# Optimization experiments

Measured on AMD Instinct MI355X. Metric: run time of the kernel, lower is better.

The kernel has to match this reference:

```python
import jax, jax.numpy as jnp
import numpy as np

E = 1024
H = 16
D = E // H  # head_dim = 64
B = 2
S = 2048


def setup_inputs() -> dict:
    key = jax.random.key(0)
    ks = jax.random.split(key, 8)
    sc = 0.02
    return {
        "x": jax.random.normal(ks[0], (B, S, E), jnp.float32),
        "rotation_params": jax.random.normal(ks[1], (E, E), jnp.float32) * sc,
        "entangle_params": jax.random.normal(ks[2], (E, E), jnp.float32) * sc,
        "qkv_w": jax.random.normal(ks[3], (3 * E, E), jnp.float32) * sc,
        "qkv_b": jax.random.normal(ks[4], (3 * E,), jnp.float32) * sc,
        "out_w": jax.random.normal(ks[5], (E, E), jnp.float32) * sc,
        "out_b": jax.random.normal(ks[6], (E,), jnp.float32) * sc,
    }


def reference(x, rotation_params, entangle_params, qkv_w, qkv_b, out_w, out_b):
    b, s, _ = x.shape
    # qkv projection (torch Linear: x @ W.T + b)
    qkv = jnp.einsum('bse,fe->bsf', x, qkv_w) + qkv_b
    q, k, v = jnp.split(qkv, 3, axis=-1)
    # extra rotation / entangle matmuls on q and k
    q = jnp.matmul(q, rotation_params)
    k = jnp.matmul(k, entangle_params)
    # split heads: (b, h, s, d)
    q = q.reshape(b, s, H, D).transpose(0, 2, 1, 3)
    k = k.reshape(b, s, H, D).transpose(0, 2, 1, 3)
    v = v.reshape(b, s, H, D).transpose(0, 2, 1, 3)
    scores = jnp.einsum('bhqd,bhkd->bhqk', q, k) / np.sqrt(D).astype(np.float32)
    attn = jax.nn.softmax(scores, axis=-1)  # dropout p=0.0 -> identity
    out = jnp.einsum('bhqk,bhkd->bhqd', attn, v)
    out = out.transpose(0, 2, 1, 3).reshape(b, s, E)
    out = jnp.einsum('bse,fe->bsf', out, out_w) + out_b
    return out + x
```

## Files before the change

kernel.cpp:

```cpp
#include <hip/hip_runtime.h>

#define US unsigned short
#define UC unsigned char

typedef __bf16 bf16x8 __attribute__((ext_vector_type(8)));
typedef float f32x4 __attribute__((ext_vector_type(4)));
typedef unsigned int u32x4 __attribute__((ext_vector_type(4)));
typedef unsigned short u16x4 __attribute__((ext_vector_type(4)));
typedef unsigned int uint2v __attribute__((ext_vector_type(2)));

#define ALPHA_Q 0.180336880111f

#if __has_builtin(__builtin_amdgcn_exp2f)
#define EXP2F(x) __builtin_amdgcn_exp2f(x)
#else
#define EXP2F(x) __expf(0.69314718f * (x))
#endif

static __device__ __forceinline__ US f2bf(float f) {
    union { float f; unsigned u; } v; v.f = f;
    unsigned r = v.u + 0x7fffu + ((v.u >> 16) & 1u);
    return (US)(r >> 16);
}
static __device__ __forceinline__ float bf2f(US h) {
    union { unsigned u; float f; } v; v.u = ((unsigned)h) << 16;
    return v.f;
}
static __device__ __forceinline__ f32x4 mfma16(bf16x8 a, bf16x8 b, f32x4 c) {
    return __builtin_amdgcn_mfma_f32_16x16x32_bf16(a, b, c, 0, 0, 0);
}
static __device__ __forceinline__ f32x4 mfma_fp8(long long a, long long b, f32x4 c) {
    return __builtin_amdgcn_mfma_f32_16x16x32_fp8_fp8(a, b, c, 0, 0, 0);
}
static __device__ __forceinline__ void gload16(const US* g, US* l) {
    __builtin_amdgcn_global_load_lds(
        (const __attribute__((address_space(1))) void*)g,
        (__attribute__((address_space(3))) void*)l, 16, 0, 0);
}
static __device__ __forceinline__ void gload16b(const UC* g, UC* l) {
    __builtin_amdgcn_global_load_lds(
        (const __attribute__((address_space(1))) void*)g,
        (__attribute__((address_space(3))) void*)l, 16, 0, 0);
}
static __device__ __forceinline__ void stf(float* p, float v) { *p = v; }
static __device__ __forceinline__ void stf(US* p, float v) { *p = f2bf(v); }

__global__ __launch_bounds__(256) void prep(
    const float* __restrict__ x, US* __restrict__ xb,
    const float* __restrict__ qkvw, US* __restrict__ wv,
    const float* __restrict__ outw, US* __restrict__ wo,
    const float* __restrict__ Rm, US* __restrict__ rt,
    const float* __restrict__ Em, US* __restrict__ et,
    US* __restrict__ wqT, US* __restrict__ wkT,
    const float* __restrict__ qkvb, float* __restrict__ b3)
{
    __shared__ float t[64][65];
    const int bx = blockIdx.x;
    if (bx < 6144) {
        int i = bx * 256 + threadIdx.x;
        const float* s; US* d; int j;
        if (i < 1048576) { s = x; d = xb; j = i; }
        else if (i < 1310720) { s = qkvw + (size_t)2048 * 1024; d = wv; j = i - 1048576; }
        else { s = outw; d = wo; j = i - 1310720; }
        f32x4 v = ((const f32x4*)s)[j];
        u16x4 o;
        o.x = f2bf(v.x); o.y = f2bf(v.y); o.z = f2bf(v.z); o.w = f2bf(v.w);
        ((u16x4*)d)[j] = o;
    } else if (bx < 7168) {
        int r = bx - 6144;
        int z = r >> 8, xy = r & 255, tbx = xy & 15, tby = xy >> 4;
        const float* ip; US* op;
        switch (z) {
            case 0: ip = Rm; op = rt; break;
            case 1: ip = Em; op = et; break;
            case 2: ip = qkvw; op = wqT; break;
            default: ip = qkvw + (size_t)1024 * 1024; op = wkT; break;
        }
        int bc = tbx * 64, br = tby * 64;
        int lx = threadIdx.x & 63, y4 = threadIdx.x >> 6;
#pragma unroll
        for (int i = 0; i < 16; ++i) {
            int rr = i * 4 + y4;
            t[rr][lx] = ip[(size_t)(br + rr) * 1024 + bc + lx];
        }
        __syncthreads();
#pragma unroll
        for (int i = 0; i < 16; ++i) {
            int c = i * 4 + y4;
            op[(size_t)(bc + c) * 1024 + br + lx] = f2bf(t[lx][c]);
        }
    } else if (bx < 7296) {
        float (*red)[64] = (float(*)[64])t;
        const int bb = bx - 7168;
        const int tid = threadIdx.x, wave = tid >> 6, lane = tid & 63;
        const int nc = bb & 31, jc = bb >> 5;
        const int n0 = nc * 64, n = n0 + lane;
        const float* M = (n0 < 1024) ? Rm : Em;
        const float* bv = qkvb + ((n0 < 1024) ? 0 : 1024);
        const int nn = (n0 < 1024) ? n : n - 1024;
        float s = 0.f;
        const int j0 = jc * 256 + wave * 64;
#pragma unroll 8
        for (int j = 0; j < 64; ++j)
            s += bv[j0 + j] * M[(size_t)(j0 + j) * 1024 + nn];
        red[wave][lane] = s;
        __syncthreads();
        if (wave == 0) {
            float tt = red[0][lane] + red[1][lane] + red[2][lane] + red[3][lane];
            atomicAdd(&b3[n], (n0 < 1024) ? tt * ALPHA_Q : tt);
        }
    } else {
        int i = (bx - 7296) * 256 + threadIdx.x;
        b3[2048 + i] = qkvb[2048 + i];
    }
}

template <typename TO>
__global__ __launch_bounds__(256) void gemm_nt64(
    const US* __restrict__ A, const US* __restrict__ Bm,
    TO* __restrict__ C, const float* __restrict__ bias,
    const float* __restrict__ resid,
    int M, int N, int K, int lda, int ldb, int ldc)
{
    __shared__ __align__(16) US sA[64 * 64];
    __shared__ __align__(16) US sB[128 * 64];
    const int tid = threadIdx.x;
    const int wave = tid >> 6, lane = tid & 63;
    const int r16 = lane & 15, q4 = lane >> 4;
    const int wm = (wave >> 1) * 32, wn = (wave & 1) * 64;
    const int c7 = r16 & 7;

    const int l8 = lane >> 3, lg = (lane & 7) ^ l8;
    const US* aptr = A + (size_t)(blockIdx.x * 64 + wave * 16 + l8) * lda + lg * 8;
    const US* bptr = Bm + (size_t)(blockIdx.y * 128 + wave * 32 + l8) * ldb + lg * 8;

    f32x4 acc[2][4];
#pragma unroll
    for (int i = 0; i < 2; ++i)
#pragma unroll
        for (int j = 0; j < 4; ++j) acc[i][j] = (f32x4){0.f, 0.f, 0.f, 0.f};

    for (int k0 = 0; k0 < K; k0 += 64) {
        gload16(aptr + k0, sA + (wave * 16) * 64);
        gload16(aptr + (size_t)8 * lda + k0, sA + (wave * 16 + 8) * 64);
#pragma unroll
        for (int c = 0; c < 4; ++c)
            gload16(bptr + (size_t)(c * 8) * ldb + k0, sB + (wave * 32 + c * 8) * 64);
        __syncthreads();
        bf16x8 af[2][2], bfr[4][2];
#pragma unroll
        for (int i = 0; i < 2; ++i)
#pragma unroll
            for (int hf = 0; hf < 2; ++hf)
                af[i][hf] = *(const bf16x8*)&sA[(wm + i * 16 + r16) * 64 + ((hf * 4 + q4) ^ c7) * 8];
#pragma unroll
        for (int j = 0; j < 4; ++j)
#pragma unroll
            for (int hf = 0; hf < 2; ++hf)
                bfr[j][hf] = *(const bf16x8*)&sB[(wn + j * 16 + r16) * 64 + ((hf * 4 + q4) ^ c7) * 8];
#pragma unroll
        for (int i = 0; i < 2; ++i)
#pragma unroll
            for (int j = 0; j < 4; ++j) {
                acc[i][j] = mfma16(af[i][0], bfr[j][0], acc[i][j]);
                acc[i][j] = mfma16(af[i][1], bfr[j][1], acc[i][j]);
            }
        __syncthreads();
    }

#pragma unroll
    for (int j = 0; j < 4; ++j) {
        int col = blockIdx.y * 128 + wn + j * 16 + r16;
        float bv = bias ? bias[col] : 0.f;
#pragma unroll
        for (int i = 0; i < 2; ++i) {
#pragma unroll
            for (int rr = 0; rr < 4; ++rr) {
                int row = blockIdx.x * 64 + wm + i * 16 + q4 * 4 + rr;
                float v = acc[i][j][rr] + bv;
                if (resid) v += resid[(size_t)row * ldc + col];
                stf(&C[(size_t)row * ldc + col], v);
            }
        }
    }
}

__global__ __launch_bounds__(256) void gemm_qkv(
    const US* __restrict__ A, const US* __restrict__ Bm,
    const float* __restrict__ bias,
    US* __restrict__ qk, UC* __restrict__ vt)
{
    __shared__ __align__(16) US sA[64 * 64];
    __shared__ __align__(16) US sB[128 * 64];
    const int tid = threadIdx.x;
    const int wave = tid >> 6, lane = tid & 63;
    const int r16 = lane & 15, q4 = lane >> 4;
    const int wm = (wave >> 1) * 32, wn = (wave & 1) * 64;
    const int c7 = r16 & 7;

    const int l8 = lane >> 3, lg = (lane & 7) ^ l8;
    const US* aptr = A + (size_t)(blockIdx.x * 64 + wave * 16 + l8) * 1024 + lg * 8;
    const US* bptr = Bm + (size_t)(blockIdx.y * 128 + wave * 32 + l8) * 1024 + lg * 8;

    f32x4 acc[2][4];
#pragma unroll
    for (int i = 0; i < 2; ++i)
#pragma unroll
        for (int j = 0; j < 4; ++j) acc[i][j] = (f32x4){0.f, 0.f, 0.f, 0.f};

    for (int k0 = 0; k0 < 1024; k0 += 64) {
        gload16(aptr + k0, sA + (wave * 16) * 64);
        gload16(aptr + (size_t)8 * 1024 + k0, sA + (wave * 16 + 8) * 64);
#pragma unroll
        for (int c = 0; c < 4; ++c)
            gload16(bptr + (size_t)(c * 8) * 1024 + k0, sB + (wave * 32 + c * 8) * 64);
        __syncthreads();
        bf16x8 af[2][2], bfr[4][2];
#pragma unroll
        for (int i = 0; i < 2; ++i)
#pragma unroll
            for (int hf = 0; hf < 2; ++hf)
                af[i][hf] = *(const bf16x8*)&sA[(wm + i * 16 + r16) * 64 + ((hf * 4 + q4) ^ c7) * 8];
#pragma unroll
        for (int j = 0; j < 4; ++j)
#pragma unroll
            for (int hf = 0; hf < 2; ++hf)
                bfr[j][hf] = *(const bf16x8*)&sB[(wn + j * 16 + r16) * 64 + ((hf * 4 + q4) ^ c7) * 8];
#pragma unroll
        for (int i = 0; i < 2; ++i)
#pragma unroll
            for (int j = 0; j < 4; ++j) {
                acc[i][j] = mfma16(af[i][0], bfr[j][0], acc[i][j]);
                acc[i][j] = mfma16(af[i][1], bfr[j][1], acc[i][j]);
            }
        __syncthreads();
    }

    if (blockIdx.y < 16) {
#pragma unroll
        for (int j = 0; j < 4; ++j) {
            int col = blockIdx.y * 128 + wn + j * 16 + r16;
            float bv = bias[col];
#pragma unroll
            for (int i = 0; i < 2; ++i)
#pragma unroll
                for (int rr = 0; rr < 4; ++rr) {
                    int row = blockIdx.x * 64 + wm + i * 16 + q4 * 4 + rr;
                    qk[(size_t)row * 2048 + col] = f2bf(acc[i][j][rr] + bv);
                }
        }
    } else {
#pragma unroll
        for (int j = 0; j < 4; ++j) {
            int col = blockIdx.y * 128 + wn + j * 16 + r16;
            float bv = bias[col];
            int f = col - 2048;
#pragma unroll
            for (int i = 0; i < 2; ++i) {
                int row0 = blockIdx.x * 64 + wm + i * 16 + q4 * 4;
                int b = row0 >> 11, s0 = row0 & 2047;
                int k = s0 & 63;
                int p = (s0 & ~63) | ((k & 24) << 1) | ((k & 32) >> 2) | (k & 7);
                int dw = __builtin_amdgcn_cvt_pk_fp8_f32(
                    acc[i][j][0] + bv, acc[i][j][1] + bv, 0, false);
                dw = __builtin_amdgcn_cvt_pk_fp8_f32(
                    acc[i][j][2] + bv, acc[i][j][3] + bv, dw, true);
                *(unsigned int*)&vt[((size_t)(b * 1024 + f)) * 2048 + p] = (unsigned)dw;
            }
        }
    }
}

__global__ __launch_bounds__(256) void gemm_fold(
    const US* __restrict__ rt, const US* __restrict__ wqT,
    const US* __restrict__ et, const US* __restrict__ wkT,
    US* __restrict__ comb)
{
    __shared__ __align__(16) US sA[64 * 32];
    __shared__ __align__(16) US sB[64 * 32];
    const US* A; const US* Bm; US* C; float alpha;
    if (blockIdx.z == 0) { A = rt; Bm = wqT; C = comb; alpha = ALPHA_Q; }
    else { A = et; Bm = wkT; C = comb + (size_t)1024 * 1024; alpha = 1.0f; }

    const int tid = threadIdx.x;
    const int wave = tid >> 6, lane = tid & 63;
    const int r16 = lane & 15, q4 = lane >> 4;
    const int wm = (wave >> 1) * 32, wn = (wave & 1) * 32;

    const int srow = wave * 16 + (lane >> 2);
    const int sg = lane & 3;
    const US* aptr = A + (size_t)(blockIdx.x * 64 + srow) * 1024 + sg * 8;
    const US* bptr = Bm + (size_t)(blockIdx.y * 64 + srow) * 1024 + sg * 8;
    US* lA = sA + (wave * 16) * 32;
    US* lB = sB + (wave * 16) * 32;

    f32x4 acc[2][2];
#pragma unroll
    for (int i = 0; i < 2; ++i)
#pragma unroll
        for (int j = 0; j < 2; ++j) acc[i][j] = (f32x4){0.f, 0.f, 0.f, 0.f};

    for (int k0 = 0; k0 < 1024; k0 += 32) {
        gload16(aptr + k0, lA);
        gload16(bptr + k0, lB);
        __syncthreads();
        bf16x8 af[2], bfr[2];
#pragma unroll
        for (int i = 0; i < 2; ++i)
            af[i] = *(const bf16x8*)&sA[(wm + i * 16 + r16) * 32 + q4 * 8];
#pragma unroll
        for (int j = 0; j < 2; ++j)
            bfr[j] = *(const bf16x8*)&sB[(wn + j * 16 + r16) * 32 + q4 * 8];
#pragma unroll
        for (int i = 0; i < 2; ++i)
#pragma unroll
            for (int j = 0; j < 2; ++j) acc[i][j] = mfma16(af[i], bfr[j], acc[i][j]);
        __syncthreads();
    }

#pragma unroll
    for (int j = 0; j < 2; ++j) {
        int col = blockIdx.y * 64 + wn + j * 16 + r16;
#pragma unroll
        for (int i = 0; i < 2; ++i)
#pragma unroll
            for (int rr = 0; rr < 4; ++rr) {
                int row = blockIdx.x * 64 + wm + i * 16 + q4 * 4 + rr;
                C[(size_t)row * 1024 + col] = f2bf(acc[i][j][rr] * alpha);
            }
    }
}

__global__ __launch_bounds__(256) void attn_kernel(
    const US* __restrict__ qk, const UC* __restrict__ vt, US* __restrict__ out)
{
    __shared__ __align__(16) US sK[2 * 64 * 64];
    __shared__ __align__(16) UC sV[2 * 64 * 64];
    __shared__ __align__(16) UC sPw[4 * 16 * 72];
    const int tid = threadIdx.x;
    const int wave = tid >> 6, lane = tid & 63;
    const int r16 = lane & 15, q4 = lane >> 4;
    const int bid = blockIdx.x;
    const int pair = (bid & 7) * 4 + ((bid >> 3) & 3);
    const int qc = bid >> 5;
    const int h = pair & 15, b = pair >> 4;
    const int qrow0 = qc * 64;
    const int c7 = r16 & 7;
    const long long ones8 = 0x3838383838383838LL;

    const US* qbase = qk + ((size_t)(b * 2048 + qrow0 + wave * 16 + r16)) * 2048 + h * 64;
    const bf16x8 qf0 = *(const bf16x8*)(qbase + q4 * 8);
    const bf16x8 qf1 = *(const bf16x8*)(qbase + 32 + q4 * 8);

    f32x4 o[4];
    f32x4 lC;
#pragma unroll
    for (int dt = 0; dt < 4; ++dt) o[dt] = (f32x4){0.f, 0.f, 0.f, 0.f};
    lC = (f32x4){0.f, 0.f, 0.f, 0.f};

    const int l8 = lane >> 3;
    const US* kg = qk + ((size_t)(b * 2048 + wave * 16 + l8)) * 2048 + 1024 + h * 64
                 + ((lane & 7) ^ l8) * 8;
    const int r4 = lane >> 2;
    const UC* vg = vt + ((size_t)((b * 16 + h) * 64 + wave * 16 + r4)) * 2048
                 + ((lane & 3) ^ (r4 & 3)) * 16;

    UC* Pw = sPw + wave * (16 * 72);
    UC* pwr = Pw + r16 * 72 + q4 * 4;
    const UC* prd = Pw + r16 * 72 + q4 * 8;

#define STAGE(kc, buf) do {                                                    \
        US* dK = sK + (buf) * 4096 + (wave * 16) * 64;                         \
        UC* dV = sV + (buf) * 4096 + (wave * 16) * 64;                         \
        gload16(kg + (size_t)(kc) * 2048, dK);                                 \
        gload16(kg + (size_t)((kc) + 8) * 2048, dK + 8 * 64);                  \
        gload16b(vg + (kc), dV);                                               \
    } while (0)

    STAGE(0, 0);
    __syncthreads();
    for (int it = 0; it < 32; ++it) {
        const int buf = it & 1;
        if (it < 31) STAGE((it + 1) * 64, buf ^ 1);
        const US* K0 = sK + buf * 4096;
        const UC* V0 = sV + buf * 4096;

#pragma unroll
        for (int kt = 0; kt < 4; ++kt) {
            bf16x8 kf0 = *(const bf16x8*)&K0[(kt * 16 + r16) * 64 + ((0 + q4) ^ c7) * 8];
            bf16x8 kf1 = *(const bf16x8*)&K0[(kt * 16 + r16) * 64 + ((4 + q4) ^ c7) * 8];
            f32x4 st = mfma16(kf0, qf0, (f32x4){0.f, 0.f, 0.f, 0.f});
            st = mfma16(kf1, qf1, st);
            float p0 = EXP2F(st[0]), p1 = EXP2F(st[1]);
            float p2 = EXP2F(st[2]), p3 = EXP2F(st[3]);
            int dw = __builtin_amdgcn_cvt_pk_fp8_f32(p0, p1, 0, false);
            dw = __builtin_amdgcn_cvt_pk_fp8_f32(p2, p3, dw, true);
            *(unsigned int*)(pwr + kt * 16) = (unsigned)dw;
        }

        u32x4 vv0 = *(const u32x4*)&V0[(0 * 16 + r16) * 64 + (q4 ^ (r16 & 3)) * 16];
        u32x4 vv1 = *(const u32x4*)&V0[(1 * 16 + r16) * 64 + (q4 ^ (r16 & 3)) * 16];
        u32x4 vv2 = *(const u32x4*)&V0[(2 * 16 + r16) * 64 + (q4 ^ (r16 & 3)) * 16];
        u32x4 vv3 = *(const u32x4*)&V0[(3 * 16 + r16) * 64 + (q4 ^ (r16 & 3)) * 16];

        asm volatile("s_waitcnt lgkmcnt(0)" ::: "memory");
        __builtin_amdgcn_sched_barrier(0);

        long long pb0 = *(const long long*)(prd);
        long long pb1 = *(const long long*)(prd + 32);

#define PVD(vvr, dt) do {                                                      \
        long long vf0, vf1;                                                    \
        { uint2v t0 = {(vvr).x, (vvr).y}; vf0 = *(long long*)&t0; }            \
        { uint2v t1 = {(vvr).z, (vvr).w}; vf1 = *(long long*)&t1; }            \
        o[dt] = mfma_fp8(vf0, pb0, o[dt]);                                     \
        o[dt] = mfma_fp8(vf1, pb1, o[dt]);                                     \
    } while (0)
        PVD(vv0, 0); PVD(vv1, 1); PVD(vv2, 2); PVD(vv3, 3);
#undef PVD
        lC = mfma_fp8(ones8, pb0, lC);
        lC = mfma_fp8(ones8, pb1, lC);

        __syncthreads();
    }
#undef STAGE

    float inv = 1.0f / lC[0];
    size_t row = (size_t)(b * 2048 + qrow0 + wave * 16 + r16);
#pragma unroll
    for (int dt = 0; dt < 4; ++dt) {
        uint2v w;
        w.x = (unsigned)f2bf(o[dt][0] * inv) | ((unsigned)f2bf(o[dt][1] * inv) << 16);
        w.y = (unsigned)f2bf(o[dt][2] * inv) | ((unsigned)f2bf(o[dt][3] * inv) << 16);
        *(uint2v*)&out[row * 1024 + h * 64 + dt * 16 + q4 * 4] = w;
    }
}

extern "C" void kernel_launch(void* const* d_in, const int* in_sizes, int n_in,
                              void* d_out, int out_size, void* d_ws, size_t ws_size,
                              hipStream_t stream)
{
    const float* x    = (const float*)d_in[0];
    const float* Rm   = (const float*)d_in[1];
    const float* Em   = (const float*)d_in[2];
    const float* qkvw = (const float*)d_in[3];
    const float* qkvb = (const float*)d_in[4];
    const float* outw = (const float*)d_in[5];
    const float* outb = (const float*)d_in[6];
    float* outp = (float*)d_out;

    US* ws    = (US*)d_ws;
    US* xb    = ws;
    US* rt    = xb   + (size_t)4096 * 1024;
    US* et    = rt   + (size_t)1024 * 1024;
    US* wqT   = et   + (size_t)1024 * 1024;
    US* wkT   = wqT  + (size_t)1024 * 1024;
    US* wo    = wkT  + (size_t)1024 * 1024;
    US* comb  = wo   + (size_t)1024 * 1024;
    US* qkvq  = comb + (size_t)3072 * 1024;
    US* ao    = qkvq + (size_t)4096 * 2048;
    UC* vt    = (UC*)(ao + (size_t)4096 * 1024);
    float* b3 = (float*)(vt + (size_t)2048 * 2048);

    hipMemsetAsync(b3, 0, 2048 * sizeof(float), stream);
    prep<<<dim3(7300), dim3(256), 0, stream>>>(
        x, xb, qkvw, comb + (size_t)2048 * 1024, outw, wo,
        Rm, rt, Em, et, wqT, wkT, qkvb, b3);
    gemm_fold<<<dim3(16, 16, 2), dim3(256), 0, stream>>>(rt, wqT, et, wkT, comb);
    gemm_qkv<<<dim3(64, 24), dim3(256), 0, stream>>>(xb, comb, b3, qkvq, vt);
    attn_kernel<<<dim3(1024), dim3(256), 0, stream>>>(qkvq, vt, ao);
    gemm_nt64<float><<<dim3(64, 8), dim3(256), 0, stream>>>(ao, wo, outp, outb, x,
                                                            4096, 1024, 1024, 1024, 1024, 1024);
}
```

Baseline: 215.0 us.

## Split attention KV range across two blocks and add combine kernel; widen fold GEMM K-tile

The attention kernel now splits each query tile's 2048 keys into two halves handled by separate blocks. Each block writes an unnormalized fp16 partial output and a row sum, and a new combine kernel adds the halves and normalizes to bf16. This doubles the grid to give more parallelism on the many-CU GPU. The cost is an extra launch, extra fp16 partial traffic, and a max-free softmax whose fp16 partials could overflow. Separately, the fold GEMM uses a 64-wide K tile with XOR-swizzled LDS, which halves the barrier count per K.

```diff
diff --git a/kernel.cpp b/kernel.cpp
--- a/kernel.cpp
+++ b/kernel.cpp
@@ -276,8 +276,8 @@
     const US* __restrict__ et, const US* __restrict__ wkT,
     US* __restrict__ comb)
 {
-    __shared__ __align__(16) US sA[64 * 32];
-    __shared__ __align__(16) US sB[64 * 32];
+    __shared__ __align__(16) US sA[64 * 64];
+    __shared__ __align__(16) US sB[64 * 64];
     const US* A; const US* Bm; US* C; float alpha;
     if (blockIdx.z == 0) { A = rt; Bm = wqT; C = comb; alpha = ALPHA_Q; }
     else { A = et; Bm = wkT; C = comb + (size_t)1024 * 1024; alpha = 1.0f; }
@@ -286,13 +286,11 @@
     const int wave = tid >> 6, lane = tid & 63;
     const int r16 = lane & 15, q4 = lane >> 4;
     const int wm = (wave >> 1) * 32, wn = (wave & 1) * 32;
-
-    const int srow = wave * 16 + (lane >> 2);
-    const int sg = lane & 3;
-    const US* aptr = A + (size_t)(blockIdx.x * 64 + srow) * 1024 + sg * 8;
-    const US* bptr = Bm + (size_t)(blockIdx.y * 64 + srow) * 1024 + sg * 8;
-    US* lA = sA + (wave * 16) * 32;
-    US* lB = sB + (wave * 16) * 32;
+    const int c7 = r16 & 7;
+
+    const int l8 = lane >> 3, lg = (lane & 7) ^ l8;
+    const US* aptr = A + (size_t)(blockIdx.x * 64 + wave * 16 + l8) * 1024 + lg * 8;
+    const US* bptr = Bm + (size_t)(blockIdx.y * 64 + wave * 16 + l8) * 1024 + lg * 8;
 
     f32x4 acc[2][2];
 #pragma unroll
@@ -300,21 +298,30 @@
 #pragma unroll
         for (int j = 0; j < 2; ++j) acc[i][j] = (f32x4){0.f, 0.f, 0.f, 0.f};
 
-    for (int k0 = 0; k0 < 1024; k0 += 32) {
-        gload16(aptr + k0, lA);
-        gload16(bptr + k0, lB);
-        __syncthreads();
-        bf16x8 af[2], bfr[2];
-#pragma unroll
-        for (int i = 0; i < 2; ++i)
-            af[i] = *(const bf16x8*)&sA[(wm + i * 16 + r16) * 32 + q4 * 8];
+    for (int k0 = 0; k0 < 1024; k0 += 64) {
+        gload16(aptr + k0, sA + (wave * 16) * 64);
+        gload16(aptr + (size_t)8 * 1024 + k0, sA + (wave * 16 + 8) * 64);
+        gload16(bptr + k0, sB + (wave * 16) * 64);
+        gload16(bptr + (size_t)8 * 1024 + k0, sB + (wave * 16 + 8) * 64);
+        __syncthreads();
+        bf16x8 af[2][2], bfr[2][2];
+#pragma unroll
+        for (int i = 0; i < 2; ++i)
+#pragma unroll
+            for (int hf = 0; hf < 2; ++hf)
+                af[i][hf] = *(const bf16x8*)&sA[(wm + i * 16 + r16) * 64 + ((hf * 4 + q4) ^ c7) * 8];
 #pragma unroll
         for (int j = 0; j < 2; ++j)
-            bfr[j] = *(const bf16x8*)&sB[(wn + j * 16 + r16) * 32 + q4 * 8];
-#pragma unroll
-        for (int i = 0; i < 2; ++i)
-#pragma unroll
-            for (int j = 0; j < 2; ++j) acc[i][j] = mfma16(af[i], bfr[j], acc[i][j]);
+#pragma unroll
+            for (int hf = 0; hf < 2; ++hf)
+                bfr[j][hf] = *(const bf16x8*)&sB[(wn + j * 16 + r16) * 64 + ((hf * 4 + q4) ^ c7) * 8];
+#pragma unroll
+        for (int i = 0; i < 2; ++i)
+#pragma unroll
+            for (int j = 0; j < 2; ++j) {
+                acc[i][j] = mfma16(af[i][0], bfr[j][0], acc[i][j]);
+                acc[i][j] = mfma16(af[i][1], bfr[j][1], acc[i][j]);
+            }
         __syncthreads();
     }
 
@@ -332,7 +339,8 @@
 }
 
 __global__ __launch_bounds__(256) void attn_kernel(
-    const US* __restrict__ qk, const UC* __restrict__ vt, US* __restrict__ out)
+    const US* __restrict__ qk, const UC* __restrict__ vt,
+    _Float16* __restrict__ po, float* __restrict__ pl)
 {
     __shared__ __align__(16) US sK[2 * 64 * 64];
     __shared__ __align__(16) UC sV[2 * 64 * 64];
@@ -341,11 +349,14 @@
     const int wave = tid >> 6, lane = tid & 63;
     const int r16 = lane & 15, q4 = lane >> 4;
     const int bid = blockIdx.x;
-    const int pair = (bid & 7) * 4 + ((bid >> 3) & 3);
-    const int qc = bid >> 5;
+    const int sp = bid & 1;
+    const int bid2 = bid >> 1;
+    const int pair = (bid2 & 7) * 4 + ((bid2 >> 3) & 3);
+    const int qc = bid2 >> 5;
     const int h = pair & 15, b = pair >> 4;
     const int qrow0 = qc * 64;
     const int c7 = r16 & 7;
+    const int kb0 = sp * 1024;
     const long long ones8 = 0x3838383838383838LL;
 
     const US* qbase = qk + ((size_t)(b * 2048 + qrow0 + wave * 16 + r16)) * 2048 + h * 64;
@@ -377,11 +388,11 @@
         gload16b(vg + (kc), dV);                                               \
     } while (0)
 
-    STAGE(0, 0);
+    STAGE(kb0, 0);
     __syncthreads();
-    for (int it = 0; it < 32; ++it) {
+    for (int it = 0; it < 16; ++it) {
         const int buf = it & 1;
-        if (it < 31) STAGE((it + 1) * 64, buf ^ 1);
+        if (it < 15) STAGE(kb0 + (it + 1) * 64, buf ^ 1);
         const US* K0 = sK + buf * 4096;
         const UC* V0 = sV + buf * 4096;
 
@@ -425,15 +436,38 @@
     }
 #undef STAGE
 
-    float inv = 1.0f / lC[0];
-    size_t row = (size_t)(b * 2048 + qrow0 + wave * 16 + r16);
+    const size_t row = (size_t)(b * 2048 + qrow0 + wave * 16 + r16);
+    if (q4 == 0) pl[(size_t)sp * 4096 + row] = lC[0];
+    _Float16* pob = po + ((size_t)sp * 4096 + row) * 1024 + h * 64;
 #pragma unroll
     for (int dt = 0; dt < 4; ++dt) {
-        uint2v w;
-        w.x = (unsigned)f2bf(o[dt][0] * inv) | ((unsigned)f2bf(o[dt][1] * inv) << 16);
-        w.y = (unsigned)f2bf(o[dt][2] * inv) | ((unsigned)f2bf(o[dt][3] * inv) << 16);
-        *(uint2v*)&out[row * 1024 + h * 64 + dt * 16 + q4 * 4] = w;
-    }
+        union { _Float16 h4[4]; uint2v u; } pk_;
+        pk_.h4[0] = (_Float16)o[dt][0];
+        pk_.h4[1] = (_Float16)o[dt][1];
+        pk_.h4[2] = (_Float16)o[dt][2];
+        pk_.h4[3] = (_Float16)o[dt][3];
+        *(uint2v*)&pob[dt * 16 + q4 * 4] = pk_.u;
+    }
+}
+
+__global__ __launch_bounds__(256) void combine(
+    const _Float16* __restrict__ po, const float* __restrict__ pl,
+    US* __restrict__ ao)
+{
+    const int row = blockIdx.x;
+    const float inv = 1.0f / (pl[row] + pl[4096 + row]);
+    const int c = threadIdx.x * 4;
+    union { uint2v u; _Float16 h4[4]; } a, bq;
+    a.u  = *(const uint2v*)&po[(size_t)row * 1024 + c];
+    bq.u = *(const uint2v*)&po[((size_t)4096 + row) * 1024 + c];
+    uint2v w;
+    US w0 = f2bf(((float)a.h4[0] + (float)bq.h4[0]) * inv);
+    US w1 = f2bf(((float)a.h4[1] + (float)bq.h4[1]) * inv);
+    US w2 = f2bf(((float)a.h4[2] + (float)bq.h4[2]) * inv);
+    US w3 = f2bf(((float)a.h4[3] + (float)bq.h4[3]) * inv);
+    w.x = (unsigned)w0 | ((unsigned)w1 << 16);
+    w.y = (unsigned)w2 | ((unsigned)w3 << 16);
+    *(uint2v*)&ao[(size_t)row * 1024 + c] = w;
 }
 
 extern "C" void kernel_launch(void* const* d_in, const int* in_sizes, int n_in,
@@ -461,6 +495,8 @@
     US* ao    = qkvq + (size_t)4096 * 2048;
     UC* vt    = (UC*)(ao + (size_t)4096 * 1024);
     float* b3 = (float*)(vt + (size_t)2048 * 2048);
+    _Float16* po = (_Float16*)(b3 + 4096);
+    float* pl = (float*)(po + (size_t)2 * 4096 * 1024);
 
     hipMemsetAsync(b3, 0, 2048 * sizeof(float), stream);
     prep<<<dim3(7300), dim3(256), 0, stream>>>(
@@ -468,7 +504,8 @@
         Rm, rt, Em, et, wqT, wkT, qkvb, b3);
     gemm_fold<<<dim3(16, 16, 2), dim3(256), 0, stream>>>(rt, wqT, et, wkT, comb);
     gemm_qkv<<<dim3(64, 24), dim3(256), 0, stream>>>(xb, comb, b3, qkvq, vt);
-    attn_kernel<<<dim3(1024), dim3(256), 0, stream>>>(qkvq, vt, ao);
+    attn_kernel<<<dim3(2048), dim3(256), 0, stream>>>(qkvq, vt, po, pl);
+    combine<<<dim3(4096), dim3(256), 0, stream>>>(po, pl, ao);
     gemm_nt64<float><<<dim3(64, 8), dim3(256), 0, stream>>>(ao, wo, outp, outb, x,
                                                             4096, 1024, 1024, 1024, 1024, 1024);
 }
```

Result: no change. 215.6 us (+0.3%).

## Double-buffer LDS tiles in GEMM kernels and widen fold kernel K-step

Applied to the files above, without the earlier changes.

Adds double-buffered shared-memory staging to the three GEMM kernels. Each iteration now prefetches the next K tile into the alternate buffer before computing on the current one, which removes one barrier per iteration and lets global loads overlap MFMA work. The fold kernel also moves from a 32-wide to a 64-wide K step and uses the XOR-swizzled layout already used by the other GEMMs. Shared memory per block doubles, which may reduce occupancy.

```diff
diff --git a/kernel.cpp b/kernel.cpp
--- a/kernel.cpp
+++ b/kernel.cpp
@@ -122,8 +122,8 @@
     const float* __restrict__ resid,
     int M, int N, int K, int lda, int ldb, int ldc)
 {
-    __shared__ __align__(16) US sA[64 * 64];
-    __shared__ __align__(16) US sB[128 * 64];
+    __shared__ __align__(16) US sA[2 * 64 * 64];
+    __shared__ __align__(16) US sB[2 * 128 * 64];
     const int tid = threadIdx.x;
     const int wave = tid >> 6, lane = tid & 63;
     const int r16 = lane & 15, q4 = lane >> 4;
@@ -140,24 +140,34 @@
 #pragma unroll
         for (int j = 0; j < 4; ++j) acc[i][j] = (f32x4){0.f, 0.f, 0.f, 0.f};
 
+#define STAGE_NT(buf, k0) do {                                                 \
+        US* dA = sA + (buf) * 4096;                                            \
+        US* dB = sB + (buf) * 8192;                                            \
+        gload16(aptr + (k0), dA + (wave * 16) * 64);                           \
+        gload16(aptr + (size_t)8 * lda + (k0), dA + (wave * 16 + 8) * 64);     \
+        _Pragma("unroll")                                                      \
+        for (int c = 0; c < 4; ++c)                                            \
+            gload16(bptr + (size_t)(c * 8) * ldb + (k0), dB + (wave * 32 + c * 8) * 64); \
+    } while (0)
+
+    STAGE_NT(0, 0);
+    __syncthreads();
     for (int k0 = 0; k0 < K; k0 += 64) {
-        gload16(aptr + k0, sA + (wave * 16) * 64);
-        gload16(aptr + (size_t)8 * lda + k0, sA + (wave * 16 + 8) * 64);
-#pragma unroll
-        for (int c = 0; c < 4; ++c)
-            gload16(bptr + (size_t)(c * 8) * ldb + k0, sB + (wave * 32 + c * 8) * 64);
-        __syncthreads();
+        const int buf = (k0 >> 6) & 1;
+        if (k0 + 64 < K) STAGE_NT(buf ^ 1, k0 + 64);
+        const US* Ab = sA + buf * 4096;
+        const US* Bb = sB + buf * 8192;
         bf16x8 af[2][2], bfr[4][2];
 #pragma unroll
         for (int i = 0; i < 2; ++i)
 #pragma unroll
             for (int hf = 0; hf < 2; ++hf)
-                af[i][hf] = *(const bf16x8*)&sA[(wm + i * 16 + r16) * 64 + ((hf * 4 + q4) ^ c7) * 8];
+                af[i][hf] = *(const bf16x8*)&Ab[(wm + i * 16 + r16) * 64 + ((hf * 4 + q4) ^ c7) * 8];
 #pragma unroll
         for (int j = 0; j < 4; ++j)
 #pragma unroll
             for (int hf = 0; hf < 2; ++hf)
-                bfr[j][hf] = *(const bf16x8*)&sB[(wn + j * 16 + r16) * 64 + ((hf * 4 + q4) ^ c7) * 8];
+                bfr[j][hf] = *(const bf16x8*)&Bb[(wn + j * 16 + r16) * 64 + ((hf * 4 + q4) ^ c7) * 8];
 #pragma unroll
         for (int i = 0; i < 2; ++i)
 #pragma unroll
@@ -167,6 +177,7 @@
             }
         __syncthreads();
     }
+#undef STAGE_NT
 
 #pragma unroll
     for (int j = 0; j < 4; ++j) {
@@ -190,8 +201,8 @@
     const float* __restrict__ bias,
     US* __restrict__ qk, UC* __restrict__ vt)
 {
-    __shared__ __align__(16) US sA[64 * 64];
-    __shared__ __align__(16) US sB[128 * 64];
+    __shared__ __align__(16) US sA[2 * 64 * 64];
+    __shared__ __align__(16) US sB[2 * 128 * 64];
     const int tid = threadIdx.x;
     const int wave = tid >> 6, lane = tid & 63;
     const int r16 = lane & 15, q4 = lane >> 4;
@@ -208,24 +219,34 @@
 #pragma unroll
         for (int j = 0; j < 4; ++j) acc[i][j] = (f32x4){0.f, 0.f, 0.f, 0.f};
 
+#define STAGE_QKV(buf, k0) do {                                                \
+        US* dA = sA + (buf) * 4096;                                            \
+        US* dB = sB + (buf) * 8192;                                            \
+        gload16(aptr + (k0), dA + (wave * 16) * 64);                           \
+        gload16(aptr + (size_t)8 * 1024 + (k0), dA + (wave * 16 + 8) * 64);    \
+        _Pragma("unroll")                                                      \
+        for (int c = 0; c < 4; ++c)                                            \
+            gload16(bptr + (size_t)(c * 8) * 1024 + (k0), dB + (wave * 32 + c * 8) * 64); \
+    } while (0)
+
+    STAGE_QKV(0, 0);
+    __syncthreads();
     for (int k0 = 0; k0 < 1024; k0 += 64) {
-        gload16(aptr + k0, sA + (wave * 16) * 64);
-        gload16(aptr + (size_t)8 * 1024 + k0, sA + (wave * 16 + 8) * 64);
-#pragma unroll
-        for (int c = 0; c < 4; ++c)
-            gload16(bptr + (size_t)(c * 8) * 1024 + k0, sB + (wave * 32 + c * 8) * 64);
-        __syncthreads();
+        const int buf = (k0 >> 6) & 1;
+        if (k0 < 960) STAGE_QKV(buf ^ 1, k0 + 64);
+        const US* Ab = sA + buf * 4096;
+        const US* Bb = sB + buf * 8192;
         bf16x8 af[2][2], bfr[4][2];
 #pragma unroll
         for (int i = 0; i < 2; ++i)
 #pragma unroll
             for (int hf = 0; hf < 2; ++hf)
-                af[i][hf] = *(const bf16x8*)&sA[(wm + i * 16 + r16) * 64 + ((hf * 4 + q4) ^ c7) * 8];
+                af[i][hf] = *(const bf16x8*)&Ab[(wm + i * 16 + r16) * 64 + ((hf * 4 + q4) ^ c7) * 8];
 #pragma unroll
         for (int j = 0; j < 4; ++j)
 #pragma unroll
             for (int hf = 0; hf < 2; ++hf)
-                bfr[j][hf] = *(const bf16x8*)&sB[(wn + j * 16 + r16) * 64 + ((hf * 4 + q4) ^ c7) * 8];
+                bfr[j][hf] = *(const bf16x8*)&Bb[(wn + j * 16 + r16) * 64 + ((hf * 4 + q4) ^ c7) * 8];
 #pragma unroll
         for (int i = 0; i < 2; ++i)
 #pragma unroll
@@ -235,6 +256,7 @@
             }
         __syncthreads();
     }
+#undef STAGE_QKV
 
     if (blockIdx.y < 16) {
 #pragma unroll
@@ -276,8 +298,8 @@
     const US* __restrict__ et, const US* __restrict__ wkT,
     US* __restrict__ comb)
 {
-    __shared__ __align__(16) US sA[64 * 32];
-    __shared__ __align__(16) US sB[64 * 32];
+    __shared__ __align__(16) US sA[2 * 64 * 64];
+    __shared__ __align__(16) US sB[2 * 64 * 64];
     const US* A; const US* Bm; US* C; float alpha;
     if (blockIdx.z == 0) { A = rt; Bm = wqT; C = comb; alpha = ALPHA_Q; }
     else { A = et; Bm = wkT; C = comb + (size_t)1024 * 1024; alpha = 1.0f; }
@@ -286,13 +308,11 @@
     const int wave = tid >> 6, lane = tid & 63;
     const int r16 = lane & 15, q4 = lane >> 4;
     const int wm = (wave >> 1) * 32, wn = (wave & 1) * 32;
-
-    const int srow = wave * 16 + (lane >> 2);
-    const int sg = lane & 3;
-    const US* aptr = A + (size_t)(blockIdx.x * 64 + srow) * 1024 + sg * 8;
-    const US* bptr = Bm + (size_t)(blockIdx.y * 64 + srow) * 1024 + sg * 8;
-    US* lA = sA + (wave * 16) * 32;
-    US* lB = sB + (wave * 16) * 32;
+    const int c7 = r16 & 7;
+
+    const int l8 = lane >> 3, lg = (lane & 7) ^ l8;
+    const US* aptr = A + (size_t)(blockIdx.x * 64 + wave * 16 + l8) * 1024 + lg * 8;
+    const US* bptr = Bm + (size_t)(blockIdx.y * 64 + wave * 16 + l8) * 1024 + lg * 8;
 
     f32x4 acc[2][2];
 #pragma unroll
@@ -300,23 +320,43 @@
 #pragma unroll
         for (int j = 0; j < 2; ++j) acc[i][j] = (f32x4){0.f, 0.f, 0.f, 0.f};
 
-    for (int k0 = 0; k0 < 1024; k0 += 32) {
-        gload16(aptr + k0, lA);
-        gload16(bptr + k0, lB);
+#define STAGE_F(buf, k0) do {                                                  \
+        US* dA = sA + (buf) * 4096;                                            \
+        US* dB = sB + (buf) * 4096;                                            \
+        gload16(aptr + (k0), dA + (wave * 16) * 64);                           \
+        gload16(aptr + (size_t)8 * 1024 + (k0), dA + (wave * 16 + 8) * 64);    \
+        gload16(bptr + (k0), dB + (wave * 16) * 64);                           \
+        gload16(bptr + (size_t)8 * 1024 + (k0), dB + (wave * 16 + 8) * 64);    \
+    } while (0)
+
+    STAGE_F(0, 0);
+    __syncthreads();
+    for (int k0 = 0; k0 < 1024; k0 += 64) {
+        const int buf = (k0 >> 6) & 1;
+        if (k0 < 960) STAGE_F(buf ^ 1, k0 + 64);
+        const US* Ab = sA + buf * 4096;
+        const US* Bb = sB + buf * 4096;
+        bf16x8 af[2][2], bfr[2][2];
+#pragma unroll
+        for (int i = 0; i < 2; ++i)
+#pragma unroll
+            for (int hf = 0; hf < 2; ++hf)
+                af[i][hf] = *(const bf16x8*)&Ab[(wm + i * 16 + r16) * 64 + ((hf * 4 + q4) ^ c7) * 8];
+#pragma unroll
+        for (int j = 0; j < 2; ++j)
+#pragma unroll
+            for (int hf = 0; hf < 2; ++hf)
+                bfr[j][hf] = *(const bf16x8*)&Bb[(wn + j * 16 + r16) * 64 + ((hf * 4 + q4) ^ c7) * 8];
+#pragma unroll
+        for (int i = 0; i < 2; ++i)
+#pragma unroll
+            for (int j = 0; j < 2; ++j) {
+                acc[i][j] = mfma16(af[i][0], bfr[j][0], acc[i][j]);
+                acc[i][j] = mfma16(af[i][1], bfr[j][1], acc[i][j]);
+            }
         __syncthreads();
-        bf16x8 af[2], bfr[2];
-#pragma unroll
-        for (int i = 0; i < 2; ++i)
-            af[i] = *(const bf16x8*)&sA[(wm + i * 16 + r16) * 32 + q4 * 8];
-#pragma unroll
-        for (int j = 0; j < 2; ++j)
-            bfr[j] = *(const bf16x8*)&sB[(wn + j * 16 + r16) * 32 + q4 * 8];
-#pragma unroll
-        for (int i = 0; i < 2; ++i)
-#pragma unroll
-            for (int j = 0; j < 2; ++j) acc[i][j] = mfma16(af[i], bfr[j], acc[i][j]);
-        __syncthreads();
-    }
+    }
+#undef STAGE_F
 
 #pragma unroll
     for (int j = 0; j < 2; ++j) {
```

Result: slower. 220.9 us (+2.7%).
